# Optimization experiments

Measured on AMD Instinct MI355X. Metric: run time of the kernel, lower is better.

The kernel has to match this reference:

```python
import jax, jax.numpy as jnp
import numpy as np

EMBED = 768
HEADS = 12
HEAD_DIM = EMBED // HEADS


def setup_inputs() -> dict:
    key = jax.random.key(0)
    ks = jax.random.split(key, 7)
    B, S = 4, 2048
    scale = 1.0 / np.sqrt(EMBED)
    return {
        "q": jax.random.normal(ks[0], (B, S, EMBED), dtype=jnp.float32),
        "k": jax.random.normal(ks[1], (B, S, EMBED), dtype=jnp.float32),
        "v": jax.random.normal(ks[2], (B, S, EMBED), dtype=jnp.float32),
        # NOTE: original torch code applies self.query to q, k AND v (bug kept faithfully),
        # so only the query projection and the output projection participate.
        "Wq": (jax.random.normal(ks[3], (EMBED, EMBED), dtype=jnp.float32) * scale),
        "bq": jnp.zeros((EMBED,), dtype=jnp.float32),
        "Wo": (jax.random.normal(ks[4], (EMBED, EMBED), dtype=jnp.float32) * scale),
        "bo": jnp.zeros((EMBED,), dtype=jnp.float32),
    }


def _split_heads(x):
    B, S, _ = x.shape
    return x.reshape(B, S, HEADS, HEAD_DIM).transpose(0, 2, 1, 3)  # [B,H,S,D]


def reference(q, k, v, Wq, bq, Wo, bo):
    # All three streams go through the *query* projection (faithful to source bug).
    qh = _split_heads(q @ Wq.T + bq)
    kh = _split_heads(k @ Wq.T + bq)
    vh = _split_heads(v @ Wq.T + bq)
    scores = jnp.einsum("bhsd,bhtd->bhst", qh, kh) / np.sqrt(HEAD_DIM)  # [B,H,S,S]
    attn = jax.nn.softmax(scores, axis=-1)  # dropout = identity (eval mode)
    out = jnp.einsum("bhst,bhtd->bhsd", attn, vh)  # [B,H,S,D]
    B, H, S, D = out.shape
    out = out.transpose(0, 2, 1, 3).reshape(B, S, H * D)  # [B,S,E]
    return out @ Wo.T + bo
```

## Files before the change

kernel.cpp:

```cpp
#include <hip/hip_runtime.h>

typedef unsigned int  uint32;
typedef unsigned short ushort_t;

using s16x8 = __attribute__((ext_vector_type(8))) short;
using bf8v  = __attribute__((ext_vector_type(8))) __bf16;
using f16x4 = __attribute__((ext_vector_type(4))) _Float16;
using f16x8 = __attribute__((ext_vector_type(8))) _Float16;
using f32x4 = __attribute__((ext_vector_type(4))) float;

typedef __attribute__((address_space(1))) void as1_void;
typedef __attribute__((address_space(3))) void as3_void;

__device__ __forceinline__ void gld16(const void* g, void* l) {
  __builtin_amdgcn_global_load_lds((const as1_void*)g, (as3_void*)l, 16, 0, 0);
}

__device__ __forceinline__ f32x4 mfma32(s16x8 a, s16x8 b, f32x4 c) {
  return __builtin_amdgcn_mfma_f32_16x16x32_bf16(
      __builtin_bit_cast(bf8v, a), __builtin_bit_cast(bf8v, b), c, 0, 0, 0);
}
__device__ __forceinline__ f32x4 mfma32h(f16x8 a, f16x8 b, f32x4 c) {
  return __builtin_amdgcn_mfma_f32_16x16x32_f16(a, b, c, 0, 0, 0);
}

__device__ __forceinline__ ushort_t f2bf(float f) {
  uint32 u = __float_as_uint(f);
  u += 0x7FFFu + ((u >> 16) & 1u);
  return (ushort_t)(u >> 16);
}
__device__ __forceinline__ f16x4 exp_pack(f32x4 st) {
  float e0 = __builtin_amdgcn_exp2f(st[0]);
  float e1 = __builtin_amdgcn_exp2f(st[1]);
  float e2 = __builtin_amdgcn_exp2f(st[2]);
  float e3 = __builtin_amdgcn_exp2f(st[3]);
  uint2 u = {__builtin_bit_cast(uint32, __builtin_amdgcn_cvt_pkrtz(e0, e1)),
             __builtin_bit_cast(uint32, __builtin_amdgcn_cvt_pkrtz(e2, e3))};
  return __builtin_bit_cast(f16x4, u);
}

__global__ __launch_bounds__(256) void cvt_all(const float* __restrict__ q,
                                               const float* __restrict__ k,
                                               const float* __restrict__ v,
                                               const float* __restrict__ Wq,
                                               const float* __restrict__ Wo,
                                               ushort_t* qb, ushort_t* kb, ushort_t* vb,
                                               ushort_t* wqb, ushort_t* wob) {
  int i = blockIdx.x * 256 + threadIdx.x;
  const float* s; ushort_t* d; int off;
  if (i < 4718592) {
    int st = i / 1572864; off = i - st * 1572864;
    s = st == 0 ? q : (st == 1 ? k : v);
    d = st == 0 ? qb : (st == 1 ? kb : vb);
  } else {
    int j = i - 4718592; int st = j / 147456; off = j - st * 147456;
    s = st ? Wo : Wq; d = st ? wob : wqb;
  }
  float4 f = ((const float4*)s)[off];
  ushort4 o = {f2bf(f.x), f2bf(f.y), f2bf(f.z), f2bf(f.w)};
  ((ushort4*)d)[off] = o;
}

__device__ __forceinline__ void gemm_core(const ushort_t* __restrict__ A,
                                          const ushort_t* __restrict__ Bw,
                                          ushort_t* As, ushort_t* Bs,
                                          int m0, int n0, f32x4 (&acc)[4][4]) {
  const int tid = threadIdx.x;
  const int wave = tid >> 6, lane = tid & 63;
  const int qd = lane >> 4, c = lane & 15;
  const int wm = wave >> 1, wn = wave & 1;
  const int pc0 = qd ^ (c & 7), pc1 = (4 + qd) ^ (c & 7);
  int row[4], cl[4], lb[4];
#pragma unroll
  for (int i = 0; i < 4; ++i) {
    int s = i * 256 + wave * 64 + lane;
    row[i] = s >> 3; cl[i] = (s & 7) ^ (row[i] & 7);
    lb[i] = (i * 256 + wave * 64) * 16;
  }
  for (int kt = 0; kt < 12; ++kt) {
    __syncthreads();
#pragma unroll
    for (int i = 0; i < 4; ++i) {
      gld16(A + (size_t)(m0 + row[i]) * 768 + kt * 64 + cl[i] * 8, (char*)As + lb[i]);
      gld16(Bw + (size_t)(n0 + row[i]) * 768 + kt * 64 + cl[i] * 8, (char*)Bs + lb[i]);
    }
    __syncthreads();
#pragma unroll
    for (int kk = 0; kk < 2; ++kk) {
      const int pcr = kk ? pc1 : pc0;
      s16x8 a[4], b[4];
#pragma unroll
      for (int i = 0; i < 4; ++i) a[i] = *(const s16x8*)(As + (wm * 64 + i * 16 + c) * 64 + pcr * 8);
#pragma unroll
      for (int j = 0; j < 4; ++j) b[j] = *(const s16x8*)(Bs + (wn * 64 + j * 16 + c) * 64 + pcr * 8);
#pragma unroll
      for (int i = 0; i < 4; ++i)
#pragma unroll
        for (int j = 0; j < 4; ++j) acc[i][j] = mfma32(a[i], b[j], acc[i][j]);
    }
  }
}

__global__ __launch_bounds__(256) void gemm_proj(const ushort_t* __restrict__ qb,
                                                 const ushort_t* __restrict__ kb,
                                                 const ushort_t* __restrict__ vb,
                                                 const ushort_t* __restrict__ Wqb,
                                                 const float* __restrict__ bias,
                                                 ushort_t* __restrict__ qh,
                                                 ushort_t* __restrict__ kh,
                                                 ushort_t* __restrict__ vt) {
  __shared__ __align__(16) ushort_t As[8192];
  __shared__ __align__(16) ushort_t Bs[8192];
  const int bz = blockIdx.z;
  const ushort_t* A = bz == 0 ? qb : (bz == 1 ? kb : vb);
  const int m0 = blockIdx.y * 128, n0 = blockIdx.x * 128;
  f32x4 acc[4][4] = {};
  gemm_core(A, Wqb, As, Bs, m0, n0, acc);
  const int tid = threadIdx.x, wave = tid >> 6, lane = tid & 63;
  const int qd = lane >> 4, c = lane & 15;
  const int wm = wave >> 1, wn = wave & 1;
  if (bz == 2) {
    const int sbase = m0 & 2047, bb = m0 >> 11;
#pragma unroll
    for (int p = 0; p < 2; ++p) {
      __syncthreads();
      if (wn == p) {
#pragma unroll
        for (int j = 0; j < 4; ++j) {
          int n64 = j * 16 + c;
          float bv = bias[n0 + p * 64 + n64];
#pragma unroll
          for (int i = 0; i < 4; ++i) {
            int ps8 = (wm * 16 + i * 4 + qd) ^ ((c & 7) << 2);
            uint2 w = {__builtin_bit_cast(uint32, __builtin_amdgcn_cvt_pkrtz(acc[i][j][0] + bv, acc[i][j][1] + bv)),
                       __builtin_bit_cast(uint32, __builtin_amdgcn_cvt_pkrtz(acc[i][j][2] + bv, acc[i][j][3] + bv))};
            *(uint2*)(As + n64 * 128 + ps8 * 4) = w;
          }
        }
      }
      __syncthreads();
      const int h = (n0 >> 6) + p;
#pragma unroll
      for (int e = 0; e < 4; ++e) {
        int ch = e * 256 + tid;
        int n64 = ch >> 4, u = ch & 15;
        uint4 w = *(const uint4*)(As + n64 * 128 + (u ^ ((n64 & 7) << 1)) * 8);
        *(uint4*)(vt + ((size_t)(bb * 12 + h) * 64 + n64) * 2048 + sbase + u * 8) = w;
      }
    }
  } else {
    ushort_t* dst = bz == 0 ? qh : kh;
    const float qsc = bz == 0 ? 0.18033688011112042f : 1.0f;
#pragma unroll
    for (int j = 0; j < 4; ++j) {
      int n = n0 + wn * 64 + j * 16 + c;
      float bv = bias[n];
      int h = n >> 6, d = n & 63;
#pragma unroll
      for (int i = 0; i < 4; ++i)
#pragma unroll
        for (int r = 0; r < 4; ++r) {
          int m = m0 + wm * 64 + i * 16 + qd * 4 + r;
          int bb = m >> 11, s = m & 2047;
          dst[((size_t)((bb * 12 + h) * 2048 + s)) * 64 + d] = f2bf((acc[i][j][r] + bv) * qsc);
        }
    }
  }
}

__global__ __launch_bounds__(256) void gemm_final(const ushort_t* __restrict__ A,
                                                  const ushort_t* __restrict__ Wob,
                                                  const float* __restrict__ bias,
                                                  float* __restrict__ out) {
  __shared__ __align__(16) ushort_t As[4096];
  __shared__ __align__(16) ushort_t Bs[8192];
  const int m0 = blockIdx.y * 64, n0 = blockIdx.x * 128;
  const int tid = threadIdx.x;
  const int wave = tid >> 6, lane = tid & 63;
  const int qd = lane >> 4, c = lane & 15;
  const int wm = wave >> 1, wn = wave & 1;
  const int pc0 = qd ^ (c & 7), pc1 = (4 + qd) ^ (c & 7);
  f32x4 acc[2][4] = {};
  int arow[2], acl[2], alb[2], brow[4], bcl[4], blb[4];
#pragma unroll
  for (int i = 0; i < 2; ++i) {
    int s = i * 256 + tid;
    arow[i] = s >> 3; acl[i] = (s & 7) ^ (arow[i] & 7);
    alb[i] = (i * 256 + wave * 64) * 16;
  }
#pragma unroll
  for (int i = 0; i < 4; ++i) {
    int s = i * 256 + tid;
    brow[i] = s >> 3; bcl[i] = (s & 7) ^ (brow[i] & 7);
    blb[i] = (i * 256 + wave * 64) * 16;
  }
  for (int kt = 0; kt < 12; ++kt) {
    __syncthreads();
#pragma unroll
    for (int i = 0; i < 2; ++i)
      gld16(A + (size_t)(m0 + arow[i]) * 768 + kt * 64 + acl[i] * 8, (char*)As + alb[i]);
#pragma unroll
    for (int i = 0; i < 4; ++i)
      gld16(Wob + (size_t)(n0 + brow[i]) * 768 + kt * 64 + bcl[i] * 8, (char*)Bs + blb[i]);
    __syncthreads();
#pragma unroll
    for (int kk = 0; kk < 2; ++kk) {
      const int pcr = kk ? pc1 : pc0;
      s16x8 a[2], b[4];
#pragma unroll
      for (int i = 0; i < 2; ++i) a[i] = *(const s16x8*)(As + (wm * 32 + i * 16 + c) * 64 + pcr * 8);
#pragma unroll
      for (int j = 0; j < 4; ++j) b[j] = *(const s16x8*)(Bs + (wn * 64 + j * 16 + c) * 64 + pcr * 8);
#pragma unroll
      for (int i = 0; i < 2; ++i)
#pragma unroll
        for (int j = 0; j < 4; ++j) acc[i][j] = mfma32(a[i], b[j], acc[i][j]);
    }
  }
#pragma unroll
  for (int j = 0; j < 4; ++j) {
    int n = n0 + wn * 64 + j * 16 + c;
    float bv = bias[n];
#pragma unroll
    for (int i = 0; i < 2; ++i)
#pragma unroll
      for (int r = 0; r < 4; ++r) {
        int m = m0 + wm * 32 + i * 16 + qd * 4 + r;
        out[(size_t)m * 768 + n] = acc[i][j][r] + bv;
      }
  }
}

__global__ __launch_bounds__(512, 4) void flash(const ushort_t* __restrict__ qh,
                                                const ushort_t* __restrict__ kh,
                                                const ushort_t* __restrict__ vt,
                                                ushort_t* __restrict__ attn) {
  __shared__ __align__(16) ushort_t Ks[128 * 64];
  __shared__ __align__(16) ushort_t Vts[64 * 128];
  const int bid = blockIdx.x;
  const int bh = bid % 48, qt = bid / 48;
  const int tid = threadIdx.x, wave = tid >> 6, lane = tid & 63;
  const int wq = wave >> 1, wk = wave & 1;
  const int qd = lane >> 4, c = lane & 15;
  const ushort_t* Qg = qh + (size_t)bh * 131072;
  const ushort_t* Kg = kh + (size_t)bh * 131072;
  const ushort_t* Vg = vt + (size_t)bh * 131072;
  const int sb = qt * 128 + wq * 32;

  s16x8 qf[2][2];
#pragma unroll
  for (int ts = 0; ts < 2; ++ts)
#pragma unroll
    for (int kk = 0; kk < 2; ++kk)
      qf[ts][kk] = *(const s16x8*)(Qg + (size_t)(sb + ts * 16 + c) * 64 + kk * 32 + qd * 8);

  const f32x4 z4 = {0.f, 0.f, 0.f, 0.f};
  const float FM = 12.0f;
  const f32x4 nFM = {-FM, -FM, -FM, -FM};
  f32x4 o[2][4], lacc[2];
#pragma unroll
  for (int ts = 0; ts < 2; ++ts) {
    lacc[ts] = z4;
#pragma unroll
    for (int dn = 0; dn < 4; ++dn) o[ts][dn] = z4;
  }
  f16x8 ones8;
#pragma unroll
  for (int e = 0; e < 8; ++e) ones8[e] = (_Float16)1.f;

  const int kpc0 = (qd) ^ (c & 7);
  const int kpc1 = (4 + qd) ^ (c & 7);
  const int pbase = wk * 2;

  int kgrow[2], kcl[2], vrow[2], vcl[2], lbase[2];
#pragma unroll
  for (int i = 0; i < 2; ++i) {
    int s = i * 512 + tid;
    int kr = s >> 3; kcl[i] = (s & 7) ^ (kr & 7);
    int u = kr & 31;
    kgrow[i] = (kr & ~31) | (((u >> 2) & 3) << 3) | (((u >> 4) & 1) << 2) | (u & 3);
    vrow[i] = s >> 4; vcl[i] = (s & 15) ^ (vrow[i] & 15);
    lbase[i] = (i * 512 + wave * 64) * 16;
  }

  for (int kt = 0; kt < 16; ++kt) {
    __syncthreads();
#pragma unroll
    for (int i = 0; i < 2; ++i)
      gld16(Kg + (size_t)(kt * 128 + kgrow[i]) * 64 + kcl[i] * 8, (char*)Ks + lbase[i]);
#pragma unroll
    for (int i = 0; i < 2; ++i)
      gld16(Vg + (size_t)vrow[i] * 2048 + kt * 128 + vcl[i] * 8, (char*)Vts + lbase[i]);
    __syncthreads();

#pragma unroll
    for (int pp = 0; pp < 2; ++pp) {
      const int p = pbase + pp;
      f16x4 e0[2], e1[2];
#pragma unroll
      for (int tile = 0; tile < 2; ++tile) {
        const int r = (p * 2 + tile) * 16 + c;
        s16x8 a0 = *(const s16x8*)(Ks + r * 64 + kpc0 * 8);
        s16x8 a1 = *(const s16x8*)(Ks + r * 64 + kpc1 * 8);
        __builtin_amdgcn_s_setprio(1);
        f32x4 st0 = mfma32(a0, qf[0][0], nFM);
        f32x4 st1 = mfma32(a0, qf[1][0], nFM);
        st0 = mfma32(a1, qf[0][1], st0);
        st1 = mfma32(a1, qf[1][1], st1);
        __builtin_amdgcn_s_setprio(0);
        e0[tile] = exp_pack(st0);
        e1[tile] = exp_pack(st1);
      }
      f16x8 A0 = __builtin_shufflevector(e0[0], e0[1], 0, 1, 2, 3, 4, 5, 6, 7);
      f16x8 A1 = __builtin_shufflevector(e1[0], e1[1], 0, 1, 2, 3, 4, 5, 6, 7);
      __builtin_amdgcn_s_setprio(1);
      lacc[0] = mfma32h(A0, ones8, lacc[0]);
      lacc[1] = mfma32h(A1, ones8, lacc[1]);
#pragma unroll
      for (int dn = 0; dn < 4; ++dn) {
        f16x8 vb = *(const f16x8*)(Vts + (dn * 16 + c) * 128 + ((4 * p + qd) ^ c) * 8);
        o[0][dn] = mfma32h(A0, vb, o[0][dn]);
        o[1][dn] = mfma32h(A1, vb, o[1][dn]);
      }
      __builtin_amdgcn_s_setprio(0);
    }
  }

  float* red = (float*)Ks;
  const int rbase = (wq * 64 + lane) * 21;
  const int bb = bh / 12, h = bh % 12;
#pragma unroll
  for (int ts = 0; ts < 2; ++ts) {
    __syncthreads();
    if (wk == 1) {
#pragma unroll
      for (int dn = 0; dn < 4; ++dn)
#pragma unroll
        for (int r = 0; r < 4; ++r) red[rbase + dn * 4 + r] = o[ts][dn][r];
#pragma unroll
      for (int r = 0; r < 4; ++r) red[rbase + 16 + r] = lacc[ts][r];
    }
    __syncthreads();
    if (wk == 0) {
      float l4[4];
#pragma unroll
      for (int r = 0; r < 4; ++r) l4[r] = lacc[ts][r] + red[rbase + 16 + r];
#pragma unroll
      for (int r = 0; r < 4; ++r) {
        float inv = 1.f / l4[r];
        int s = sb + ts * 16 + qd * 4 + r;
#pragma unroll
        for (int dn = 0; dn < 4; ++dn) {
          float val = (o[ts][dn][r] + red[rbase + dn * 4 + r]) * inv;
          attn[((size_t)(bb * 2048 + s)) * 768 + h * 64 + dn * 16 + c] = f2bf(val);
        }
      }
    }
  }
}

extern "C" void kernel_launch(void* const* d_in, const int* in_sizes, int n_in,
                              void* d_out, int out_size, void* d_ws, size_t ws_size,
                              hipStream_t stream) {
  const float* q  = (const float*)d_in[0];
  const float* k  = (const float*)d_in[1];
  const float* v  = (const float*)d_in[2];
  const float* Wq = (const float*)d_in[3];
  const float* bq = (const float*)d_in[4];
  const float* Wo = (const float*)d_in[5];
  const float* bo = (const float*)d_in[6];
  float* out = (float*)d_out;
  char* ws = (char*)d_ws;

  ushort_t* qbf = (ushort_t*)(ws + 0);
  ushort_t* kbf = (ushort_t*)(ws + 12582912);
  ushort_t* vbf = (ushort_t*)(ws + 25165824);
  ushort_t* wqb = (ushort_t*)(ws + 37748736);
  ushort_t* wob = (ushort_t*)(ws + 38928384);
  ushort_t* qhp = (ushort_t*)(ws + 40108032);
  ushort_t* khp = (ushort_t*)(ws + 52690944);
  ushort_t* vtp = (ushort_t*)(ws + 65273856);
  ushort_t* att = (ushort_t*)(ws + 0);

  cvt_all<<<dim3(19584), 256, 0, stream>>>(q, k, v, Wq, Wo, qbf, kbf, vbf, wqb, wob);
  gemm_proj<<<dim3(6, 64, 3), 256, 0, stream>>>(qbf, kbf, vbf, wqb, bq, qhp, khp, vtp);
  flash<<<dim3(768), 512, 0, stream>>>(qhp, khp, vtp, att);
  gemm_final<<<dim3(6, 128), 256, 0, stream>>>(att, wob, bo, out);
}
```

Measured before the change: 253.1 us.

## Double-buffer K/V tiles in LDS with smaller 64-key steps

```diff
diff --git a/kernel.cpp b/kernel.cpp
--- a/kernel.cpp
+++ b/kernel.cpp
@@ -235,8 +235,7 @@
                                                 const ushort_t* __restrict__ kh,
                                                 const ushort_t* __restrict__ vt,
                                                 ushort_t* __restrict__ attn) {
-  __shared__ __align__(16) ushort_t Ks[128 * 64];
-  __shared__ __align__(16) ushort_t Vts[64 * 128];
+  __shared__ __align__(16) ushort_t lds[16384];
   const int bid = blockIdx.x;
   const int bh = bid % 48, qt = bid / 48;
   const int tid = threadIdx.x, wave = tid >> 6, lane = tid & 63;
@@ -270,63 +269,63 @@
 
   const int kpc0 = (qd) ^ (c & 7);
   const int kpc1 = (4 + qd) ^ (c & 7);
-  const int pbase = wk * 2;
-
-  int kgrow[2], kcl[2], vrow[2], vcl[2], lbase[2];
-#pragma unroll
-  for (int i = 0; i < 2; ++i) {
-    int s = i * 512 + tid;
-    int kr = s >> 3; kcl[i] = (s & 7) ^ (kr & 7);
-    int u = kr & 31;
-    kgrow[i] = (kr & ~31) | (((u >> 2) & 3) << 3) | (((u >> 4) & 1) << 2) | (u & 3);
-    vrow[i] = s >> 4; vcl[i] = (s & 15) ^ (vrow[i] & 15);
-    lbase[i] = (i * 512 + wave * 64) * 16;
-  }
-
-  for (int kt = 0; kt < 16; ++kt) {
-    __syncthreads();
-#pragma unroll
-    for (int i = 0; i < 2; ++i)
-      gld16(Kg + (size_t)(kt * 128 + kgrow[i]) * 64 + kcl[i] * 8, (char*)Ks + lbase[i]);
-#pragma unroll
-    for (int i = 0; i < 2; ++i)
-      gld16(Vg + (size_t)vrow[i] * 2048 + kt * 128 + vcl[i] * 8, (char*)Vts + lbase[i]);
-    __syncthreads();
-
-#pragma unroll
-    for (int pp = 0; pp < 2; ++pp) {
-      const int p = pbase + pp;
-      f16x4 e0[2], e1[2];
-#pragma unroll
-      for (int tile = 0; tile < 2; ++tile) {
-        const int r = (p * 2 + tile) * 16 + c;
-        s16x8 a0 = *(const s16x8*)(Ks + r * 64 + kpc0 * 8);
-        s16x8 a1 = *(const s16x8*)(Ks + r * 64 + kpc1 * 8);
-        __builtin_amdgcn_s_setprio(1);
-        f32x4 st0 = mfma32(a0, qf[0][0], nFM);
-        f32x4 st1 = mfma32(a0, qf[1][0], nFM);
-        st0 = mfma32(a1, qf[0][1], st0);
-        st1 = mfma32(a1, qf[1][1], st1);
-        __builtin_amdgcn_s_setprio(0);
-        e0[tile] = exp_pack(st0);
-        e1[tile] = exp_pack(st1);
-      }
-      f16x8 A0 = __builtin_shufflevector(e0[0], e0[1], 0, 1, 2, 3, 4, 5, 6, 7);
-      f16x8 A1 = __builtin_shufflevector(e1[0], e1[1], 0, 1, 2, 3, 4, 5, 6, 7);
+
+  const int s0 = tid;
+  const int kr = s0 >> 3;
+  const int kcl = (s0 & 7) ^ (kr & 7);
+  const int u = kr & 31;
+  const int kgrow = (kr & ~31) | (((u >> 2) & 3) << 3) | (((u >> 4) & 1) << 2) | (u & 3);
+  const int vrow = s0 >> 3;
+  const int vcl = (s0 & 7) ^ (vrow & 7);
+  const int lbase = tid * 16;
+
+  gld16(Kg + (size_t)kgrow * 64 + kcl * 8, (char*)lds + lbase);
+  gld16(Vg + (size_t)vrow * 2048 + vcl * 8, (char*)lds + 16384 + lbase);
+  __syncthreads();
+
+  for (int kt = 0; kt < 32; ++kt) {
+    const int cur = kt & 1;
+    if (kt < 31) {
+      gld16(Kg + (size_t)((kt + 1) * 64 + kgrow) * 64 + kcl * 8,
+            (char*)lds + (cur ? 0 : 8192) + lbase);
+      gld16(Vg + (size_t)vrow * 2048 + (kt + 1) * 64 + vcl * 8,
+            (char*)lds + (cur ? 16384 : 24576) + lbase);
+    }
+    const ushort_t* Kb = lds + (cur ? 4096 : 0);
+    const ushort_t* Vb = lds + (cur ? 12288 : 8192);
+
+    f16x4 e0[2], e1[2];
+#pragma unroll
+    for (int tile = 0; tile < 2; ++tile) {
+      const int r = wk * 32 + tile * 16 + c;
+      s16x8 a0 = *(const s16x8*)(Kb + r * 64 + kpc0 * 8);
+      s16x8 a1 = *(const s16x8*)(Kb + r * 64 + kpc1 * 8);
       __builtin_amdgcn_s_setprio(1);
-      lacc[0] = mfma32h(A0, ones8, lacc[0]);
-      lacc[1] = mfma32h(A1, ones8, lacc[1]);
-#pragma unroll
-      for (int dn = 0; dn < 4; ++dn) {
-        f16x8 vb = *(const f16x8*)(Vts + (dn * 16 + c) * 128 + ((4 * p + qd) ^ c) * 8);
-        o[0][dn] = mfma32h(A0, vb, o[0][dn]);
-        o[1][dn] = mfma32h(A1, vb, o[1][dn]);
-      }
+      f32x4 st0 = mfma32(a0, qf[0][0], nFM);
+      f32x4 st1 = mfma32(a0, qf[1][0], nFM);
+      st0 = mfma32(a1, qf[0][1], st0);
+      st1 = mfma32(a1, qf[1][1], st1);
       __builtin_amdgcn_s_setprio(0);
-    }
-  }
-
-  float* red = (float*)Ks;
+      e0[tile] = exp_pack(st0);
+      e1[tile] = exp_pack(st1);
+    }
+    f16x8 A0 = __builtin_shufflevector(e0[0], e0[1], 0, 1, 2, 3, 4, 5, 6, 7);
+    f16x8 A1 = __builtin_shufflevector(e1[0], e1[1], 0, 1, 2, 3, 4, 5, 6, 7);
+    __builtin_amdgcn_s_setprio(1);
+    lacc[0] = mfma32h(A0, ones8, lacc[0]);
+    lacc[1] = mfma32h(A1, ones8, lacc[1]);
+#pragma unroll
+    for (int dn = 0; dn < 4; ++dn) {
+      f16x8 vb = *(const f16x8*)(Vb + (dn * 16 + c) * 64 + ((4 * wk + qd) ^ (c & 7)) * 8);
+      o[0][dn] = mfma32h(A0, vb, o[0][dn]);
+      o[1][dn] = mfma32h(A1, vb, o[1][dn]);
+    }
+    __builtin_amdgcn_s_setprio(0);
+
+    __syncthreads();
+  }
+
+  float* red = (float*)lds;
   const int rbase = (wq * 64 + lane) * 21;
   const int bb = bh / 12, h = bh % 12;
 #pragma unroll
```

Measured after the change: 247.8 us. 2.1% less time.
